# Kernel optimization log

Measured on AMD Instinct MI355X. Metric: run time of the kernel, lower is better.

## Reference

```python
import jax, jax.numpy as jnp
import numpy as np

DIM = 1024
HEADS = 16
HEAD_DIM = DIM // HEADS
SEQ_TGT = 2048  # query length
SEQ_SRC = 1024  # key/value length
BATCH = 4
LN_EPS = 1e-5


def setup_inputs() -> dict:
    key = jax.random.key(0)
    ks = jax.random.split(key, 8)
    s = 1.0 / np.sqrt(DIM)
    return {
        "q": jax.random.normal(ks[0], (BATCH, SEQ_TGT, DIM), dtype=jnp.float32),
        "kv": jax.random.normal(ks[1], (BATCH, SEQ_SRC, DIM), dtype=jnp.float32),
        "Wq": jax.random.normal(ks[2], (DIM, DIM), dtype=jnp.float32) * s,
        "Wk": jax.random.normal(ks[3], (DIM, DIM), dtype=jnp.float32) * s,
        "Wv": jax.random.normal(ks[4], (DIM, DIM), dtype=jnp.float32) * s,
        "Wo": jax.random.normal(ks[5], (DIM, DIM), dtype=jnp.float32) * s,
        "bo": jnp.zeros((DIM,), dtype=jnp.float32),
        "ln_g": jnp.ones((DIM,), dtype=jnp.float32),
        "ln_b": jnp.zeros((DIM,), dtype=jnp.float32),
    }


def _split_heads(x):
    b, n, _ = x.shape
    return x.reshape(b, n, HEADS, HEAD_DIM).transpose(0, 2, 1, 3)  # b h n d


def reference(q, kv, Wq, Wk, Wv, Wo, bo, ln_g, ln_b):
    # QKV projections (torch Linear: x @ W.T, no bias)
    qh = _split_heads(q @ Wq.T)    # [b,h,Nq,d]
    kh = _split_heads(kv @ Wk.T)   # [b,h,Nk,d]
    vh = _split_heads(kv @ Wv.T)   # [b,h,Nk,d]

    scale = HEAD_DIM ** -0.5
    qk = jnp.einsum('bhid,bhjd->bhij', qh, kh) * scale  # [b,h,Nq,Nk]

    # Block-causal mask: base [Nk,Nk] causal mask repeat_interleaved along query
    # axis by downscaling = Nq // Nk. Equivalent to allow iff (i // downscaling) >= j.
    downscaling = SEQ_TGT // SEQ_SRC  # = 2, upscaled_dim = 0
    i = jnp.arange(SEQ_TGT)[:, None]
    j = jnp.arange(SEQ_SRC)[None, :]
    neg_inf = jnp.asarray(-jnp.inf, dtype=qk.dtype)
    mask = jnp.where((i // downscaling) >= j, jnp.asarray(0.0, qk.dtype), neg_inf)

    attn = jax.nn.softmax(qk + mask[None, None, :, :], axis=-1)
    out = jnp.einsum('bhij,bhjd->bhid', attn, vh)           # [b,h,Nq,d]
    out = out.transpose(0, 2, 1, 3).reshape(BATCH, SEQ_TGT, DIM)

    # LayerNorm (norm_out=True)
    mu = jnp.mean(out, axis=-1, keepdims=True)
    var = jnp.mean(jnp.square(out - mu), axis=-1, keepdims=True)
    out = (out - mu) * jax.lax.rsqrt(var + LN_EPS) * ln_g + ln_b

    # Output projection (dropout is identity in eval mode)
    return out @ Wo.T + bo
```

## Files before the change

### kernel.cpp

```cpp
#include <hip/hip_runtime.h>

typedef unsigned short u16;
typedef unsigned int   u32;

typedef __bf16 bf16x8 __attribute__((ext_vector_type(8)));
typedef __bf16 bf16x4 __attribute__((ext_vector_type(4)));
typedef float  f32x4  __attribute__((ext_vector_type(4)));

__device__ __forceinline__ float bf2f(u16 v) {
    u32 u = ((u32)v) << 16; float f; __builtin_memcpy(&f, &u, 4); return f;
}
__device__ __forceinline__ u16 f2bf(float f) {
    __bf16 h = (__bf16)f; u16 r; __builtin_memcpy(&r, &h, 2); return r;
}

__device__ __forceinline__ void gload_lds16(const void* g, void* l) {
    __builtin_amdgcn_global_load_lds(
        (const __attribute__((address_space(1))) u32*)g,
        (__attribute__((address_space(3))) u32*)l, 16, 0, 0);
}

__device__ __forceinline__ void barrier_raw() {
    __builtin_amdgcn_s_barrier();
    asm volatile("" ::: "memory");
}

#define QSCALE 0.1803368801111204f

__global__ __launch_bounds__(256) void cvt_all(
    const float* __restrict__ q, const float* __restrict__ kv,
    const float* __restrict__ Wq, const float* __restrict__ Wk,
    const float* __restrict__ Wv, const float* __restrict__ Wo,
    u16* __restrict__ dst)
{
    const int total = 16 << 18;
    int i = blockIdx.x * 256 + threadIdx.x;
    const int stride = gridDim.x * 256;
    for (; i < total; i += stride) {
        int seg = i >> 18;
        const float* s; int off;
        if (seg < 8)        { s = q;  off = i; }
        else if (seg < 12)  { s = kv; off = i - (8 << 18); }
        else if (seg == 12) { s = Wq; off = i & 262143; }
        else if (seg == 13) { s = Wk; off = i & 262143; }
        else if (seg == 14) { s = Wv; off = i & 262143; }
        else                { s = Wo; off = i & 262143; }
        float4 v = reinterpret_cast<const float4*>(s)[off];
        ushort4 o;
        o.x = f2bf(v.x); o.y = f2bf(v.y); o.z = f2bf(v.z); o.w = f2bf(v.w);
        reinterpret_cast<ushort4*>(dst)[i] = o;
    }
}

template<int KK, int MH, bool RB>
__device__ __forceinline__ void qkv_phase(
    const char* ldsb, int d, int ha, int hb, int rbB, int fr, int fq,
    bf16x8 (&bF)[4], f32x4 (&acc)[8][4])
{
    const int sw = ((KK * 4 + fq) ^ (fr & 7)) * 16;
    if (RB) {
        #pragma unroll
        for (int ni = 0; ni < 4; ni++)
            bF[ni] = *reinterpret_cast<const bf16x8*>(
                ldsb + 65536 + d * 32768 + hb * 16384 + (rbB + ni * 16 + fr) * 128 + sw);
    }
    bf16x8 aF[4];
    #pragma unroll
    for (int j = 0; j < 4; j++)
        aF[j] = *reinterpret_cast<const bf16x8*>(
            ldsb + d * 32768 + ha * 16384 + ((MH * 4 + j) * 16 + fr) * 128 + sw);
    __builtin_amdgcn_s_setprio(1);
    #pragma unroll
    for (int j = 0; j < 4; j++)
        #pragma unroll
        for (int ni = 0; ni < 4; ni++)
            acc[MH * 4 + j][ni] = __builtin_amdgcn_mfma_f32_16x16x32_bf16(
                aF[j], bF[ni], acc[MH * 4 + j][ni], 0, 0, 0);
    __builtin_amdgcn_s_setprio(0);
}

__global__ __launch_bounds__(512, 2) void gemm_qkv8(
    const u16* __restrict__ q8, const u16* __restrict__ kv8,
    const u16* __restrict__ Wq8, const u16* __restrict__ Wk8,
    const u16* __restrict__ Wv8,
    u16* __restrict__ Qb, u16* __restrict__ Kb, u16* __restrict__ Vb)
{
    __shared__ __align__(16) u16 lds[65536];
    char* ldsb = (char*)lds;

    const int tid = threadIdx.x;
    const int l = tid & 63, w = tid >> 6;
    const int fr = l & 15, fq = l >> 4;

    const int bid = (int)blockIdx.x;
    const int lbid = (bid & 7) * 32 + (bid >> 3);
    const u16 *A, *W; u16* C; float scale = 1.0f; int rt, ct;
    if (lbid < 128)      { A = q8;  W = Wq8; C = Qb; scale = QSCALE; rt = lbid >> 2; ct = lbid & 3; }
    else if (lbid < 192) { int t = lbid - 128; A = kv8; W = Wk8; C = Kb; rt = t >> 2; ct = t & 3; }
    else                 { int t = lbid - 192; A = kv8; W = Wv8; C = Vb; rt = t >> 2; ct = t & 3; }
    const int brow = rt * 256, bcol = ct * 256;

    const int wr = (w >> 2) * 128, wc = (w & 3) * 64;
    const int ha = w >> 2;
    const int hb = (w & 3) >> 1;
    const int rbB = wc & 64;

    const int srow = l >> 3;
    const int sslot = (l & 7) ^ srow;

    const u16* srcA[2][2];
    const u16* srcB[2][2];
    #pragma unroll
    for (int h = 0; h < 2; h++)
        #pragma unroll
        for (int i = 0; i < 2; i++) {
            int grow = h * 128 + (2 * w + i) * 8 + srow;
            srcA[h][i] = A + (size_t)(brow + grow) * 1024 + sslot * 8;
            srcB[h][i] = W + (size_t)(bcol + grow) * 1024 + sslot * 8;
        }

    auto stageA = [&](int kt, int d) {
        #pragma unroll
        for (int h = 0; h < 2; h++)
            #pragma unroll
            for (int i = 0; i < 2; i++)
                gload_lds16(srcA[h][i] + kt * 64,
                            ldsb + d * 32768 + h * 16384 + (2 * w + i) * 1024);
    };
    auto stageBh = [&](int kt, int d, int h) {
        #pragma unroll
        for (int i = 0; i < 2; i++)
            gload_lds16(srcB[h][i] + kt * 64,
                        ldsb + 65536 + d * 32768 + h * 16384 + (2 * w + i) * 1024);
    };

    f32x4 acc[8][4] = {};

    stageA(0, 0); stageBh(0, 0, 0); stageBh(0, 0, 1);
    asm volatile("s_waitcnt vmcnt(0)" ::: "memory");
    barrier_raw();

    for (int kt = 0; kt < 16; ++kt) {
        const int d = kt & 1, nd = d ^ 1;
        const bool pre = (kt < 15);
        bf16x8 bF[4];

        if (pre) stageA(kt + 1, nd);
        qkv_phase<0, 0, true >(ldsb, d, ha, hb, rbB, fr, fq, bF, acc);
        barrier_raw();
        if (pre) stageBh(kt + 1, nd, 0);
        qkv_phase<0, 1, false>(ldsb, d, ha, hb, rbB, fr, fq, bF, acc);
        barrier_raw();
        if (pre) stageBh(kt + 1, nd, 1);
        qkv_phase<1, 0, true >(ldsb, d, ha, hb, rbB, fr, fq, bF, acc);
        barrier_raw();
        qkv_phase<1, 1, false>(ldsb, d, ha, hb, rbB, fr, fq, bF, acc);
        asm volatile("s_waitcnt vmcnt(0)" ::: "memory");
        barrier_raw();
    }

    #pragma unroll
    for (int mi = 0; mi < 8; mi++) {
        int row = brow + wr + mi * 16 + fq * 4;
        #pragma unroll
        for (int ni = 0; ni < 4; ni++) {
            int col = bcol + wc + ni * 16 + fr;
            #pragma unroll
            for (int r = 0; r < 4; r++)
                C[(size_t)(row + r) * 1024 + col] = f2bf(acc[mi][ni][r] * scale);
        }
    }
}

__global__ __launch_bounds__(512, 1) void gemm_out8(
    const u16* __restrict__ A, const u16* __restrict__ W,
    const float* __restrict__ bias, float* __restrict__ C)
{
    __shared__ __align__(16) u16 lds[49152];
    char* ldsb = (char*)lds;

    const int tid = threadIdx.x;
    const int l = tid & 63, w = tid >> 6;
    const int fr = l & 15, fq = l >> 4;

    const int bid = (int)blockIdx.x;
    const int lbid = (bid & 7) * 32 + (bid >> 3);
    const int rt = lbid >> 2, ct = lbid & 3;
    const int brow = rt * 128, bcol = ct * 256;

    const int wr = (w >> 2) * 64, wc = (w & 3) * 64;
    const int hb = (w & 3) >> 1;
    const int rbB = wc & 64;

    const int srow = l >> 3;
    const int sslot = (l & 7) ^ srow;

    const u16* srcA[2];
    const u16* srcB[2][2];
    #pragma unroll
    for (int i = 0; i < 2; i++) {
        int grow = (2 * w + i) * 8 + srow;
        srcA[i] = A + (size_t)(brow + grow) * 1024 + sslot * 8;
    }
    #pragma unroll
    for (int h = 0; h < 2; h++)
        #pragma unroll
        for (int i = 0; i < 2; i++) {
            int grow = h * 128 + (2 * w + i) * 8 + srow;
            srcB[h][i] = W + (size_t)(bcol + grow) * 1024 + sslot * 8;
        }

    auto stageA = [&](int kt, int d) {
        #pragma unroll
        for (int i = 0; i < 2; i++)
            gload_lds16(srcA[i] + kt * 64, ldsb + d * 16384 + (2 * w + i) * 1024);
    };
    auto stageB = [&](int kt, int d) {
        #pragma unroll
        for (int h = 0; h < 2; h++)
            #pragma unroll
            for (int i = 0; i < 2; i++)
                gload_lds16(srcB[h][i] + kt * 64,
                            ldsb + 32768 + d * 32768 + h * 16384 + (2 * w + i) * 1024);
    };

    f32x4 acc[4][4] = {};

    stageA(0, 0); stageB(0, 0);
    asm volatile("s_waitcnt vmcnt(0)" ::: "memory");
    barrier_raw();

    for (int kt = 0; kt < 16; ++kt) {
        const int d = kt & 1, nd = d ^ 1;
        const bool pre = (kt < 15);

        if (pre) stageA(kt + 1, nd);
        #pragma unroll
        for (int kk = 0; kk < 2; kk++) {
            const int sw = ((kk * 4 + fq) ^ (fr & 7)) * 16;
            bf16x8 aF[4], bF[4];
            #pragma unroll
            for (int j = 0; j < 4; j++)
                aF[j] = *reinterpret_cast<const bf16x8*>(
                    ldsb + d * 16384 + ((wr + j * 16 + fr) & 127) * 128 + sw);
            #pragma unroll
            for (int ni = 0; ni < 4; ni++)
                bF[ni] = *reinterpret_cast<const bf16x8*>(
                    ldsb + 32768 + d * 32768 + hb * 16384
                    + (rbB + ni * 16 + fr) * 128 + sw);
            __builtin_amdgcn_s_setprio(1);
            #pragma unroll
            for (int j = 0; j < 4; j++)
                #pragma unroll
                for (int ni = 0; ni < 4; ni++)
                    acc[j][ni] = __builtin_amdgcn_mfma_f32_16x16x32_bf16(
                        aF[j], bF[ni], acc[j][ni], 0, 0, 0);
            __builtin_amdgcn_s_setprio(0);
            if (kk == 0) {
                barrier_raw();
                if (pre) stageB(kt + 1, nd);
            }
        }
        asm volatile("s_waitcnt vmcnt(0)" ::: "memory");
        barrier_raw();
    }

    #pragma unroll
    for (int mi = 0; mi < 4; mi++) {
        int row = brow + wr + mi * 16 + fq * 4;
        #pragma unroll
        for (int ni = 0; ni < 4; ni++) {
            int col = bcol + wc + ni * 16 + fr;
            float bv = bias[col];
            #pragma unroll
            for (int r = 0; r < 4; r++)
                C[(size_t)(row + r) * 1024 + col] = acc[mi][ni][r] + bv;
        }
    }
}

__global__ __launch_bounds__(256) void attn_kernel(
    const u16* __restrict__ Q, const u16* __restrict__ K,
    const u16* __restrict__ V, u16* __restrict__ O)
{
    __shared__ __align__(16) u16 smem[25600];
    u16* Ks = smem;
    u16* Vt = smem + 8192;
    u16* Ps = smem + 16384;
    float* Ow = (float*)smem;

    const int tid = threadIdx.x;
    const int l = tid & 63, w = tid >> 6;
    const int fr = l & 15, fq = l >> 4;
    const int bh = blockIdx.y, b = bh >> 4, h = bh & 15;
    const int kp = tid & 31, d0 = (tid >> 5) * 8;
    const int kr = l >> 3, ksw = l & 7;
    u16* Pw = Ps + w * (32 * 72);

    const u16* Kbh = K + (size_t)b * 1024 * 1024 + h * 64;
    const u16* Vbh = V + (size_t)b * 1024 * 1024 + h * 64;

    for (int half = 0; half < 2; ++half) {
        const int bq = half ? (int)blockIdx.x : 15 - (int)blockIdx.x;
        const int q0 = bq * 128;

        if (half) __syncthreads();

        bf16x8 qf[2][2];
        #pragma unroll
        for (int n = 0; n < 2; n++) {
            size_t qoff = (size_t)(b * 2048 + q0 + w * 32 + n * 16 + fr) * 1024 + h * 64;
            qf[n][0] = *reinterpret_cast<const bf16x8*>(Q + qoff + fq * 8);
            qf[n][1] = *reinterpret_cast<const bf16x8*>(Q + qoff + 32 + fq * 8);
        }

        float mx[2]   = {-1e30f, -1e30f};
        float ssum[2] = {0.f, 0.f};
        f32x4 of[4][2] = {};

        {
            #pragma unroll
            for (int i = 0; i < 2; i++) {
                int cI = w * 2 + i;
                int r = cI * 8 + kr;
                gload_lds16(Kbh + (size_t)r * 1024 + ((ksw ^ (r & 7)) * 8), &Ks[cI * 512]);
            }
            const u16* vp = Vbh + (size_t)(2 * kp) * 1024 + d0;
            uint4 ra = *reinterpret_cast<const uint4*>(vp);
            uint4 rb = *reinterpret_cast<const uint4*>(vp + 1024);
            u16 ea[8], eb[8];
            __builtin_memcpy(ea, &ra, 16);
            __builtin_memcpy(eb, &rb, 16);
            #pragma unroll
            for (int jd = 0; jd < 8; jd++) {
                int d = d0 + jd;
                u32 pk = (u32)ea[jd] | ((u32)eb[jd] << 16);
                *(u32*)((char*)Vt + d * 128 + (((kp >> 2) ^ (d & 7)) * 16) + (kp & 3) * 4) = pk;
            }
        }
        __syncthreads();

        int cur = 0;
        for (int t = 0; t <= bq; ++t) {
            const bool pre = (t < bq);
            uint4 ra, rb;
            if (pre) {
                const int j0n = (t + 1) * 64;
                #pragma unroll
                for (int i = 0; i < 2; i++) {
                    int cI = w * 2 + i;
                    int r = cI * 8 + kr;
                    gload_lds16(Kbh + (size_t)(j0n + r) * 1024 + ((ksw ^ (r & 7)) * 8),
                                &Ks[(cur ^ 1) * 4096 + cI * 512]);
                }
                const u16* vp = Vbh + (size_t)(j0n + 2 * kp) * 1024 + d0;
                ra = *reinterpret_cast<const uint4*>(vp);
                rb = *reinterpret_cast<const uint4*>(vp + 1024);
            }

            f32x4 sf[4][2] = {};
            #pragma unroll
            for (int kk = 0; kk < 2; kk++) {
                bf16x8 kf[4];
                #pragma unroll
                for (int m = 0; m < 4; m++) {
                    int key = m * 16 + fr;
                    kf[m] = *reinterpret_cast<const bf16x8*>(
                        (char*)Ks + cur * 8192 + key * 128 + (((kk * 4 + fq) ^ (key & 7)) * 16));
                }
                #pragma unroll
                for (int m = 0; m < 4; m++)
                    #pragma unroll
                    for (int n = 0; n < 2; n++)
                        sf[m][n] = __builtin_amdgcn_mfma_f32_16x16x32_bf16(
                            kf[m], qf[n][kk], sf[m][n], 0, 0, 0);
            }

            const bool diag = (t == bq);
            float tmax[2] = {-1e30f, -1e30f};
            #pragma unroll
            for (int m = 0; m < 4; m++)
                #pragma unroll
                for (int n = 0; n < 2; n++)
                    #pragma unroll
                    for (int r = 0; r < 4; r++) {
                        float s = sf[m][n][r];
                        if (diag) {
                            int kl = m * 16 + fq * 4 + r;
                            int ql = w * 32 + n * 16 + fr;
                            if (kl > (ql >> 1)) s = -1e30f;
                        }
                        sf[m][n][r] = s;
                        tmax[n] = fmaxf(tmax[n], s);
                    }
            #pragma unroll
            for (int n = 0; n < 2; n++) {
                tmax[n] = fmaxf(tmax[n], __shfl_xor(tmax[n], 16));
                tmax[n] = fmaxf(tmax[n], __shfl_xor(tmax[n], 32));
            }

            const bool skip = __all(fmaxf(tmax[0] - mx[0], tmax[1] - mx[1]) <= 8.0f);
            if (!skip) {
                float al[2];
                #pragma unroll
                for (int n = 0; n < 2; n++) {
                    float mn = fmaxf(mx[n], tmax[n]);
                    al[n] = __builtin_amdgcn_exp2f(mx[n] - mn);
                    mx[n] = mn;
                    ssum[n] *= al[n];
                }
                #pragma unroll
                for (int m = 0; m < 4; m++)
                    #pragma unroll
                    for (int n = 0; n < 2; n++)
                        of[m][n] *= al[n];
            }

            float rs[2] = {0.f, 0.f};
            #pragma unroll
            for (int m = 0; m < 4; m++)
                #pragma unroll
                for (int n = 0; n < 2; n++)
                    #pragma unroll
                    for (int r = 0; r < 4; r++) {
                        float e = __builtin_amdgcn_exp2f(sf[m][n][r] - mx[n]);
                        sf[m][n][r] = e;
                        rs[n] += e;
                    }
            #pragma unroll
            for (int n = 0; n < 2; n++) {
                rs[n] += __shfl_xor(rs[n], 16);
                rs[n] += __shfl_xor(rs[n], 32);
                ssum[n] += rs[n];
            }

            #pragma unroll
            for (int m = 0; m < 4; m++)
                #pragma unroll
                for (int n = 0; n < 2; n++) {
                    bf16x4 pk;
                    pk[0] = (__bf16)sf[m][n][0]; pk[1] = (__bf16)sf[m][n][1];
                    pk[2] = (__bf16)sf[m][n][2]; pk[3] = (__bf16)sf[m][n][3];
                    int q = n * 16 + fr;
                    *(bf16x4*)((char*)Pw + q * 144 + m * 32 + fq * 8) = pk;
                }

            #pragma unroll
            for (int kk = 0; kk < 2; kk++) {
                bf16x8 pf[2], vf[4];
                #pragma unroll
                for (int n = 0; n < 2; n++) {
                    int q = n * 16 + fr;
                    pf[n] = *reinterpret_cast<const bf16x8*>(
                        (char*)Pw + q * 144 + kk * 64 + fq * 16);
                }
                #pragma unroll
                for (int m = 0; m < 4; m++) {
                    int d = m * 16 + fr;
                    vf[m] = *reinterpret_cast<const bf16x8*>(
                        (char*)Vt + cur * 8192 + d * 128 + (((kk * 4 + fq) ^ (d & 7)) * 16));
                }
                #pragma unroll
                for (int m = 0; m < 4; m++)
                    #pragma unroll
                    for (int n = 0; n < 2; n++)
                        of[m][n] = __builtin_amdgcn_mfma_f32_16x16x32_bf16(
                            vf[m], pf[n], of[m][n], 0, 0, 0);
            }

            if (pre) {
                u16 ea[8], eb[8];
                __builtin_memcpy(ea, &ra, 16);
                __builtin_memcpy(eb, &rb, 16);
                #pragma unroll
                for (int jd = 0; jd < 8; jd++) {
                    int d = d0 + jd;
                    u32 pk = (u32)ea[jd] | ((u32)eb[jd] << 16);
                    *(u32*)((char*)Vt + (cur ^ 1) * 8192 + d * 128
                            + (((kp >> 2) ^ (d & 7)) * 16) + (kp & 3) * 4) = pk;
                }
            }
            __syncthreads();
            cur ^= 1;
        }

        float* OwW = Ow + w * (32 * 68);
        #pragma unroll
        for (int m = 0; m < 4; m++)
            #pragma unroll
            for (int n = 0; n < 2; n++) {
                f32x4 v = of[m][n] * (1.0f / ssum[n]);
                int q = n * 16 + fr;
                *reinterpret_cast<f32x4*>(&OwW[q * 68 + m * 16 + fq * 4]) = v;
            }
        {
            int ql = l >> 1, dh = l & 1;
            size_t grow = (size_t)(b * 2048 + q0 + w * 32 + ql) * 1024 + h * 64 + dh * 32;
            #pragma unroll
            for (int p = 0; p < 4; p++) {
                f32x4 a = *reinterpret_cast<const f32x4*>(&OwW[ql * 68 + dh * 32 + p * 8]);
                f32x4 c = *reinterpret_cast<const f32x4*>(&OwW[ql * 68 + dh * 32 + p * 8 + 4]);
                bf16x8 pk;
                pk[0]=(__bf16)a[0]; pk[1]=(__bf16)a[1]; pk[2]=(__bf16)a[2]; pk[3]=(__bf16)a[3];
                pk[4]=(__bf16)c[0]; pk[5]=(__bf16)c[1]; pk[6]=(__bf16)c[2]; pk[7]=(__bf16)c[3];
                *reinterpret_cast<bf16x8*>(O + grow + p * 8) = pk;
            }
        }
    }
}

__global__ __launch_bounds__(256) void ln_kernel(
    u16* __restrict__ buf, const float* __restrict__ g, const float* __restrict__ beta)
{
    const int row = blockIdx.x, tid = threadIdx.x;
    const size_t base = (size_t)row * 1024;
    ushort4 v = *reinterpret_cast<const ushort4*>(&buf[base + tid * 4]);
    float x0 = bf2f(v.x), x1 = bf2f(v.y), x2 = bf2f(v.z), x3 = bf2f(v.w);
    float s = x0 + x1 + x2 + x3;
    float q = x0 * x0 + x1 * x1 + x2 * x2 + x3 * x3;
    #pragma unroll
    for (int d = 32; d; d >>= 1) { s += __shfl_xor(s, d); q += __shfl_xor(q, d); }
    __shared__ float sm[8];
    int w = tid >> 6, l = tid & 63;
    if (l == 0) { sm[w] = s; sm[4 + w] = q; }
    __syncthreads();
    s = sm[0] + sm[1] + sm[2] + sm[3];
    q = sm[4] + sm[5] + sm[6] + sm[7];
    float mean = s * (1.0f / 1024.0f);
    float var = q * (1.0f / 1024.0f) - mean * mean;
    float rstd = rsqrtf(var + 1e-5f);
    float4 gv = *reinterpret_cast<const float4*>(&g[tid * 4]);
    float4 bv = *reinterpret_cast<const float4*>(&beta[tid * 4]);
    ushort4 o;
    o.x = f2bf((x0 - mean) * rstd * gv.x + bv.x);
    o.y = f2bf((x1 - mean) * rstd * gv.y + bv.y);
    o.z = f2bf((x2 - mean) * rstd * gv.z + bv.z);
    o.w = f2bf((x3 - mean) * rstd * gv.w + bv.w);
    *reinterpret_cast<ushort4*>(&buf[base + tid * 4]) = o;
}

extern "C" void kernel_launch(void* const* d_in, const int* in_sizes, int n_in,
                              void* d_out, int out_size, void* d_ws, size_t ws_size,
                              hipStream_t stream)
{
    const float* q    = (const float*)d_in[0];
    const float* kv   = (const float*)d_in[1];
    const float* Wq   = (const float*)d_in[2];
    const float* Wk   = (const float*)d_in[3];
    const float* Wv   = (const float*)d_in[4];
    const float* Wo   = (const float*)d_in[5];
    const float* bo   = (const float*)d_in[6];
    const float* ln_g = (const float*)d_in[7];
    const float* ln_b = (const float*)d_in[8];

    const size_t MQ = (size_t)8192 * 1024;
    const size_t MK = (size_t)4096 * 1024;
    const size_t MW = (size_t)1024 * 1024;

    u16* q8  = (u16*)d_ws;
    u16* kv8 = q8 + MQ;
    u16* Wq8 = kv8 + MK;
    u16* Wk8 = Wq8 + MW;
    u16* Wv8 = Wk8 + MW;
    u16* Wo8 = Wv8 + MW;
    u16* Qb  = Wo8 + MW;
    u16* Kb  = Qb + MQ;
    u16* Vb  = Kb + MK;
    u16* Ab  = Vb + MK;

    cvt_all<<<2048, 256, 0, stream>>>(q, kv, Wq, Wk, Wv, Wo, q8);
    gemm_qkv8<<<256, 512, 0, stream>>>(q8, kv8, Wq8, Wk8, Wv8, Qb, Kb, Vb);
    attn_kernel<<<dim3(8, 64), 256, 0, stream>>>(Qb, Kb, Vb, Ab);
    ln_kernel<<<8192, 256, 0, stream>>>(Ab, ln_g, ln_b);
    gemm_out8<<<256, 512, 0, stream>>>(Ab, Wo8, bo, (float*)d_out);
}
```

Measured before the change: 129.0 us.

## Process paired high/low query tiles in one KV sweep to share K/V loads

Each attention block used to handle its two causal query tiles (high and low) one after the other, reloading K/V for the low tile. Now both tiles are processed in a single loop over KV tiles: each loaded K/V tile is consumed by the high tile and, while still within its causal range, by the low tile. This removes the repeated K/V global loads and the second loop's barriers. In exchange it holds two sets of Q fragments and accumulators in registers and uses more shared memory for a second P buffer, which may lower occupancy.

```diff
diff --git a/kernel.cpp b/kernel.cpp
--- a/kernel.cpp
+++ b/kernel.cpp
@@ -283,7 +283,7 @@
     const u16* __restrict__ Q, const u16* __restrict__ K,
     const u16* __restrict__ V, u16* __restrict__ O)
 {
-    __shared__ __align__(16) u16 smem[25600];
+    __shared__ __align__(16) u16 smem[34816];
     u16* Ks = smem;
     u16* Vt = smem + 8192;
     u16* Ps = smem + 16384;
@@ -295,39 +295,188 @@
     const int bh = blockIdx.y, b = bh >> 4, h = bh & 15;
     const int kp = tid & 31, d0 = (tid >> 5) * 8;
     const int kr = l >> 3, ksw = l & 7;
-    u16* Pw = Ps + w * (32 * 72);
+    u16* PwH = Ps + w * (32 * 72);
+    u16* PwL = Ps + (4 + w) * (32 * 72);
 
     const u16* Kbh = K + (size_t)b * 1024 * 1024 + h * 64;
     const u16* Vbh = V + (size_t)b * 1024 * 1024 + h * 64;
 
-    for (int half = 0; half < 2; ++half) {
-        const int bq = half ? (int)blockIdx.x : 15 - (int)blockIdx.x;
-        const int q0 = bq * 128;
-
-        if (half) __syncthreads();
-
-        bf16x8 qf[2][2];
+    const int x = (int)blockIdx.x;
+    const int hq = 15 - x, lq = x;
+    const int q0H = hq * 128, q0L = lq * 128;
+
+    bf16x8 qfH[2][2], qfL[2][2];
+    #pragma unroll
+    for (int n = 0; n < 2; n++) {
+        size_t qoH = (size_t)(b * 2048 + q0H + w * 32 + n * 16 + fr) * 1024 + h * 64;
+        qfH[n][0] = *reinterpret_cast<const bf16x8*>(Q + qoH + fq * 8);
+        qfH[n][1] = *reinterpret_cast<const bf16x8*>(Q + qoH + 32 + fq * 8);
+        size_t qoL = (size_t)(b * 2048 + q0L + w * 32 + n * 16 + fr) * 1024 + h * 64;
+        qfL[n][0] = *reinterpret_cast<const bf16x8*>(Q + qoL + fq * 8);
+        qfL[n][1] = *reinterpret_cast<const bf16x8*>(Q + qoL + 32 + fq * 8);
+    }
+
+    float mxH[2] = {-1e30f, -1e30f}, mxL[2] = {-1e30f, -1e30f};
+    float ssH[2] = {0.f, 0.f},       ssL[2] = {0.f, 0.f};
+    f32x4 ofH[4][2] = {}, ofL[4][2] = {};
+
+    auto process = [&](int cur, bf16x8 (&qf)[2][2], float (&mx)[2], float (&ss)[2],
+                       f32x4 (&of)[4][2], u16* Pw, bool diag) {
+        f32x4 sf[4][2] = {};
+        #pragma unroll
+        for (int kk = 0; kk < 2; kk++) {
+            bf16x8 kf[4];
+            #pragma unroll
+            for (int m = 0; m < 4; m++) {
+                int key = m * 16 + fr;
+                kf[m] = *reinterpret_cast<const bf16x8*>(
+                    (char*)Ks + cur * 8192 + key * 128 + (((kk * 4 + fq) ^ (key & 7)) * 16));
+            }
+            #pragma unroll
+            for (int m = 0; m < 4; m++)
+                #pragma unroll
+                for (int n = 0; n < 2; n++)
+                    sf[m][n] = __builtin_amdgcn_mfma_f32_16x16x32_bf16(
+                        kf[m], qf[n][kk], sf[m][n], 0, 0, 0);
+        }
+
+        float tmax[2] = {-1e30f, -1e30f};
+        #pragma unroll
+        for (int m = 0; m < 4; m++)
+            #pragma unroll
+            for (int n = 0; n < 2; n++)
+                #pragma unroll
+                for (int r = 0; r < 4; r++) {
+                    float s = sf[m][n][r];
+                    if (diag) {
+                        int kl = m * 16 + fq * 4 + r;
+                        int ql = w * 32 + n * 16 + fr;
+                        if (kl > (ql >> 1)) s = -1e30f;
+                    }
+                    sf[m][n][r] = s;
+                    tmax[n] = fmaxf(tmax[n], s);
+                }
         #pragma unroll
         for (int n = 0; n < 2; n++) {
-            size_t qoff = (size_t)(b * 2048 + q0 + w * 32 + n * 16 + fr) * 1024 + h * 64;
-            qf[n][0] = *reinterpret_cast<const bf16x8*>(Q + qoff + fq * 8);
-            qf[n][1] = *reinterpret_cast<const bf16x8*>(Q + qoff + 32 + fq * 8);
-        }
-
-        float mx[2]   = {-1e30f, -1e30f};
-        float ssum[2] = {0.f, 0.f};
-        f32x4 of[4][2] = {};
-
-        {
+            tmax[n] = fmaxf(tmax[n], __shfl_xor(tmax[n], 16));
+            tmax[n] = fmaxf(tmax[n], __shfl_xor(tmax[n], 32));
+        }
+
+        const bool skip = __all(fmaxf(tmax[0] - mx[0], tmax[1] - mx[1]) <= 8.0f);
+        if (!skip) {
+            float al[2];
+            #pragma unroll
+            for (int n = 0; n < 2; n++) {
+                float mn = fmaxf(mx[n], tmax[n]);
+                al[n] = __builtin_amdgcn_exp2f(mx[n] - mn);
+                mx[n] = mn;
+                ss[n] *= al[n];
+            }
+            #pragma unroll
+            for (int m = 0; m < 4; m++)
+                #pragma unroll
+                for (int n = 0; n < 2; n++)
+                    of[m][n] *= al[n];
+        }
+
+        float rs[2] = {0.f, 0.f};
+        #pragma unroll
+        for (int m = 0; m < 4; m++)
+            #pragma unroll
+            for (int n = 0; n < 2; n++)
+                #pragma unroll
+                for (int r = 0; r < 4; r++) {
+                    float e = __builtin_amdgcn_exp2f(sf[m][n][r] - mx[n]);
+                    sf[m][n][r] = e;
+                    rs[n] += e;
+                }
+        #pragma unroll
+        for (int n = 0; n < 2; n++) {
+            rs[n] += __shfl_xor(rs[n], 16);
+            rs[n] += __shfl_xor(rs[n], 32);
+            ss[n] += rs[n];
+        }
+
+        #pragma unroll
+        for (int m = 0; m < 4; m++)
+            #pragma unroll
+            for (int n = 0; n < 2; n++) {
+                bf16x4 pk;
+                pk[0] = (__bf16)sf[m][n][0]; pk[1] = (__bf16)sf[m][n][1];
+                pk[2] = (__bf16)sf[m][n][2]; pk[3] = (__bf16)sf[m][n][3];
+                int q = n * 16 + fr;
+                *(bf16x4*)((char*)Pw + q * 144 + m * 32 + fq * 8) = pk;
+            }
+
+        #pragma unroll
+        for (int kk = 0; kk < 2; kk++) {
+            bf16x8 pf[2], vf[4];
+            #pragma unroll
+            for (int n = 0; n < 2; n++) {
+                int q = n * 16 + fr;
+                pf[n] = *reinterpret_cast<const bf16x8*>(
+                    (char*)Pw + q * 144 + kk * 64 + fq * 16);
+            }
+            #pragma unroll
+            for (int m = 0; m < 4; m++) {
+                int d = m * 16 + fr;
+                vf[m] = *reinterpret_cast<const bf16x8*>(
+                    (char*)Vt + cur * 8192 + d * 128 + (((kk * 4 + fq) ^ (d & 7)) * 16));
+            }
+            #pragma unroll
+            for (int m = 0; m < 4; m++)
+                #pragma unroll
+                for (int n = 0; n < 2; n++)
+                    of[m][n] = __builtin_amdgcn_mfma_f32_16x16x32_bf16(
+                        vf[m], pf[n], of[m][n], 0, 0, 0);
+        }
+    };
+
+    {
+        #pragma unroll
+        for (int i = 0; i < 2; i++) {
+            int cI = w * 2 + i;
+            int r = cI * 8 + kr;
+            gload_lds16(Kbh + (size_t)r * 1024 + ((ksw ^ (r & 7)) * 8), &Ks[cI * 512]);
+        }
+        const u16* vp = Vbh + (size_t)(2 * kp) * 1024 + d0;
+        uint4 ra = *reinterpret_cast<const uint4*>(vp);
+        uint4 rb = *reinterpret_cast<const uint4*>(vp + 1024);
+        u16 ea[8], eb[8];
+        __builtin_memcpy(ea, &ra, 16);
+        __builtin_memcpy(eb, &rb, 16);
+        #pragma unroll
+        for (int jd = 0; jd < 8; jd++) {
+            int d = d0 + jd;
+            u32 pk = (u32)ea[jd] | ((u32)eb[jd] << 16);
+            *(u32*)((char*)Vt + d * 128 + (((kp >> 2) ^ (d & 7)) * 16) + (kp & 3) * 4) = pk;
+        }
+    }
+    __syncthreads();
+
+    int cur = 0;
+    for (int t = 0; t <= hq; ++t) {
+        const bool pre = (t < hq);
+        uint4 ra, rb;
+        if (pre) {
+            const int j0n = (t + 1) * 64;
             #pragma unroll
             for (int i = 0; i < 2; i++) {
                 int cI = w * 2 + i;
                 int r = cI * 8 + kr;
-                gload_lds16(Kbh + (size_t)r * 1024 + ((ksw ^ (r & 7)) * 8), &Ks[cI * 512]);
-            }
-            const u16* vp = Vbh + (size_t)(2 * kp) * 1024 + d0;
-            uint4 ra = *reinterpret_cast<const uint4*>(vp);
-            uint4 rb = *reinterpret_cast<const uint4*>(vp + 1024);
+                gload_lds16(Kbh + (size_t)(j0n + r) * 1024 + ((ksw ^ (r & 7)) * 8),
+                            &Ks[(cur ^ 1) * 4096 + cI * 512]);
+            }
+            const u16* vp = Vbh + (size_t)(j0n + 2 * kp) * 1024 + d0;
+            ra = *reinterpret_cast<const uint4*>(vp);
+            rb = *reinterpret_cast<const uint4*>(vp + 1024);
+        }
+
+        process(cur, qfH, mxH, ssH, ofH, PwH, t == hq);
+        if (t <= lq)
+            process(cur, qfL, mxL, ssL, ofL, PwL, t == lq);
+
+        if (pre) {
             u16 ea[8], eb[8];
             __builtin_memcpy(ea, &ra, 16);
             __builtin_memcpy(eb, &rb, 16);
@@ -335,161 +484,25 @@
             for (int jd = 0; jd < 8; jd++) {
                 int d = d0 + jd;
                 u32 pk = (u32)ea[jd] | ((u32)eb[jd] << 16);
-                *(u32*)((char*)Vt + d * 128 + (((kp >> 2) ^ (d & 7)) * 16) + (kp & 3) * 4) = pk;
+                *(u32*)((char*)Vt + (cur ^ 1) * 8192 + d * 128
+                        + (((kp >> 2) ^ (d & 7)) * 16) + (kp & 3) * 4) = pk;
             }
         }
         __syncthreads();
-
-        int cur = 0;
-        for (int t = 0; t <= bq; ++t) {
-            const bool pre = (t < bq);
-            uint4 ra, rb;
-            if (pre) {
-                const int j0n = (t + 1) * 64;
-                #pragma unroll
-                for (int i = 0; i < 2; i++) {
-                    int cI = w * 2 + i;
-                    int r = cI * 8 + kr;
-                    gload_lds16(Kbh + (size_t)(j0n + r) * 1024 + ((ksw ^ (r & 7)) * 8),
-                                &Ks[(cur ^ 1) * 4096 + cI * 512]);
-                }
-                const u16* vp = Vbh + (size_t)(j0n + 2 * kp) * 1024 + d0;
-                ra = *reinterpret_cast<const uint4*>(vp);
-                rb = *reinterpret_cast<const uint4*>(vp + 1024);
-            }
-
-            f32x4 sf[4][2] = {};
-            #pragma unroll
-            for (int kk = 0; kk < 2; kk++) {
-                bf16x8 kf[4];
-                #pragma unroll
-                for (int m = 0; m < 4; m++) {
-                    int key = m * 16 + fr;
-                    kf[m] = *reinterpret_cast<const bf16x8*>(
-                        (char*)Ks + cur * 8192 + key * 128 + (((kk * 4 + fq) ^ (key & 7)) * 16));
-                }
-                #pragma unroll
-                for (int m = 0; m < 4; m++)
-                    #pragma unroll
-                    for (int n = 0; n < 2; n++)
-                        sf[m][n] = __builtin_amdgcn_mfma_f32_16x16x32_bf16(
-                            kf[m], qf[n][kk], sf[m][n], 0, 0, 0);
-            }
-
-            const bool diag = (t == bq);
-            float tmax[2] = {-1e30f, -1e30f};
-            #pragma unroll
-            for (int m = 0; m < 4; m++)
-                #pragma unroll
-                for (int n = 0; n < 2; n++)
-                    #pragma unroll
-                    for (int r = 0; r < 4; r++) {
-                        float s = sf[m][n][r];
-                        if (diag) {
-                            int kl = m * 16 + fq * 4 + r;
-                            int ql = w * 32 + n * 16 + fr;
-                            if (kl > (ql >> 1)) s = -1e30f;
-                        }
-                        sf[m][n][r] = s;
-                        tmax[n] = fmaxf(tmax[n], s);
-                    }
+        cur ^= 1;
+    }
+
+    float* OwW = Ow + w * (32 * 68);
+    #pragma unroll
+    for (int c = 0; c < 2; c++) {
+        const int q0 = c ? q0L : q0H;
+        f32x4 (&of)[4][2] = c ? ofL : ofH;
+        float (&ss)[2] = c ? ssL : ssH;
+        #pragma unroll
+        for (int m = 0; m < 4; m++)
             #pragma unroll
             for (int n = 0; n < 2; n++) {
-                tmax[n] = fmaxf(tmax[n], __shfl_xor(tmax[n], 16));
-                tmax[n] = fmaxf(tmax[n], __shfl_xor(tmax[n], 32));
-            }
-
-            const bool skip = __all(fmaxf(tmax[0] - mx[0], tmax[1] - mx[1]) <= 8.0f);
-            if (!skip) {
-                float al[2];
-                #pragma unroll
-                for (int n = 0; n < 2; n++) {
-                    float mn = fmaxf(mx[n], tmax[n]);
-                    al[n] = __builtin_amdgcn_exp2f(mx[n] - mn);
-                    mx[n] = mn;
-                    ssum[n] *= al[n];
-                }
-                #pragma unroll
-                for (int m = 0; m < 4; m++)
-                    #pragma unroll
-                    for (int n = 0; n < 2; n++)
-                        of[m][n] *= al[n];
-            }
-
-            float rs[2] = {0.f, 0.f};
-            #pragma unroll
-            for (int m = 0; m < 4; m++)
-                #pragma unroll
-                for (int n = 0; n < 2; n++)
-                    #pragma unroll
-                    for (int r = 0; r < 4; r++) {
-                        float e = __builtin_amdgcn_exp2f(sf[m][n][r] - mx[n]);
-                        sf[m][n][r] = e;
-                        rs[n] += e;
-                    }
-            #pragma unroll
-            for (int n = 0; n < 2; n++) {
-                rs[n] += __shfl_xor(rs[n], 16);
-                rs[n] += __shfl_xor(rs[n], 32);
-                ssum[n] += rs[n];
-            }
-
-            #pragma unroll
-            for (int m = 0; m < 4; m++)
-                #pragma unroll
-                for (int n = 0; n < 2; n++) {
-                    bf16x4 pk;
-                    pk[0] = (__bf16)sf[m][n][0]; pk[1] = (__bf16)sf[m][n][1];
-                    pk[2] = (__bf16)sf[m][n][2]; pk[3] = (__bf16)sf[m][n][3];
-                    int q = n * 16 + fr;
-                    *(bf16x4*)((char*)Pw + q * 144 + m * 32 + fq * 8) = pk;
-                }
-
-            #pragma unroll
-            for (int kk = 0; kk < 2; kk++) {
-                bf16x8 pf[2], vf[4];
-                #pragma unroll
-                for (int n = 0; n < 2; n++) {
-                    int q = n * 16 + fr;
-                    pf[n] = *reinterpret_cast<const bf16x8*>(
-                        (char*)Pw + q * 144 + kk * 64 + fq * 16);
-                }
-                #pragma unroll
-                for (int m = 0; m < 4; m++) {
-                    int d = m * 16 + fr;
-                    vf[m] = *reinterpret_cast<const bf16x8*>(
-                        (char*)Vt + cur * 8192 + d * 128 + (((kk * 4 + fq) ^ (d & 7)) * 16));
-                }
-                #pragma unroll
-                for (int m = 0; m < 4; m++)
-                    #pragma unroll
-                    for (int n = 0; n < 2; n++)
-                        of[m][n] = __builtin_amdgcn_mfma_f32_16x16x32_bf16(
-                            vf[m], pf[n], of[m][n], 0, 0, 0);
-            }
-
-            if (pre) {
-                u16 ea[8], eb[8];
-                __builtin_memcpy(ea, &ra, 16);
-                __builtin_memcpy(eb, &rb, 16);
-                #pragma unroll
-                for (int jd = 0; jd < 8; jd++) {
-                    int d = d0 + jd;
-                    u32 pk = (u32)ea[jd] | ((u32)eb[jd] << 16);
-                    *(u32*)((char*)Vt + (cur ^ 1) * 8192 + d * 128
-                            + (((kp >> 2) ^ (d & 7)) * 16) + (kp & 3) * 4) = pk;
-                }
-            }
-            __syncthreads();
-            cur ^= 1;
-        }
-
-        float* OwW = Ow + w * (32 * 68);
-        #pragma unroll
-        for (int m = 0; m < 4; m++)
-            #pragma unroll
-            for (int n = 0; n < 2; n++) {
-                f32x4 v = of[m][n] * (1.0f / ssum[n]);
+                f32x4 v = of[m][n] * (1.0f / ss[n]);
                 int q = n * 16 + fr;
                 *reinterpret_cast<f32x4*>(&OwW[q * 68 + m * 16 + fq * 4]) = v;
             }
@@ -499,10 +512,10 @@
             #pragma unroll
             for (int p = 0; p < 4; p++) {
                 f32x4 a = *reinterpret_cast<const f32x4*>(&OwW[ql * 68 + dh * 32 + p * 8]);
-                f32x4 c = *reinterpret_cast<const f32x4*>(&OwW[ql * 68 + dh * 32 + p * 8 + 4]);
+                f32x4 cc = *reinterpret_cast<const f32x4*>(&OwW[ql * 68 + dh * 32 + p * 8 + 4]);
                 bf16x8 pk;
                 pk[0]=(__bf16)a[0]; pk[1]=(__bf16)a[1]; pk[2]=(__bf16)a[2]; pk[3]=(__bf16)a[3];
-                pk[4]=(__bf16)c[0]; pk[5]=(__bf16)c[1]; pk[6]=(__bf16)c[2]; pk[7]=(__bf16)c[3];
+                pk[4]=(__bf16)cc[0]; pk[5]=(__bf16)cc[1]; pk[6]=(__bf16)cc[2]; pk[7]=(__bf16)cc[3];
                 *reinterpret_cast<bf16x8*>(O + grow + p * 8) = pk;
             }
         }
```

Measured after the change: 152.6 us. 1.18x slower.
